# Kernel optimization log

Measured on AMD Instinct MI355X. Metric: run time of the kernel, lower is better.

Reference implementation:

```python
import jax, jax.numpy as jnp
import numpy as np

H = 16
EMB = 1024
DH = 64  # att_dim


def setup_inputs() -> dict:
    key = jax.random.key(0)
    k1, k2, k3 = jax.random.split(key, 3)
    B, T = 4, 2048
    x = jax.random.normal(k1, (B, T, EMB), dtype=jnp.float32)
    # torch nn.Linear weight layout: [out_features, in_features]
    w_qkv = jax.random.normal(k2, (3 * H * DH, EMB), dtype=jnp.float32) * (1.0 / np.sqrt(EMB))
    wo = jax.random.normal(k3, (EMB, H * DH), dtype=jnp.float32) * (1.0 / np.sqrt(H * DH))
    return {"x": x, "w_qkv": w_qkv, "wo": wo}


def reference(x, w_qkv, wo):
    B, T, C = x.shape
    qkv = jnp.einsum('btc,oc->bto', x, w_qkv)  # [B,T,3*H*DH]
    q, k, v = jnp.split(qkv, 3, axis=-1)
    # [B,H,T,DH]
    q = q.reshape(B, T, H, DH).transpose(0, 2, 1, 3)
    k = k.reshape(B, T, H, DH).transpose(0, 2, 1, 3)
    v = v.reshape(B, T, H, DH).transpose(0, 2, 1, 3)
    scale = 1.0 / np.sqrt(DH).astype(np.float32)
    scores = jnp.einsum('bhqd,bhkd->bhqk', q, k) * scale
    causal = jnp.tril(jnp.ones((T, T), dtype=bool))
    scores = jnp.where(causal, scores, jnp.finfo(scores.dtype).min)
    attn = jax.nn.softmax(scores, axis=-1)
    y = jnp.einsum('bhqk,bhkd->bhqd', attn, v)  # [B,H,T,DH]
    y = y.transpose(0, 2, 1, 3).reshape(B, T, H * DH)
    return jnp.einsum('bti,oi->bto', y, wo)
```

## Files before the change

kernel.cpp:

```cpp
#include <hip/hip_runtime.h>
#include <hip/hip_bf16.h>
#include <stdint.h>


typedef __attribute__((ext_vector_type(8))) short short8;
typedef __attribute__((ext_vector_type(4))) float floatx4;

extern "C" __device__ float __ocml_native_exp2_f32(float);

__device__ __forceinline__ ushort f2bf(float f) {
  uint32_t u = __float_as_uint(f);
  u += 0x7fff + ((u >> 16) & 1);
  return (ushort)(u >> 16);
}

#if __has_builtin(__builtin_amdgcn_cvt_pk_bf16_f32)
typedef __attribute__((ext_vector_type(2))) __bf16 bf16x2;
__device__ __forceinline__ uint32_t pack_bf16(float a, float b) {
  union { bf16x2 v; uint32_t u; } cv;
  cv.v = __builtin_amdgcn_cvt_pk_bf16_f32(a, b);
  return cv.u;
}
#else
__device__ __forceinline__ uint32_t pack_bf16(float a, float b) {
  uint32_t ua = __float_as_uint(a) + 0x8000u;
  uint32_t ub = __float_as_uint(b) + 0x8000u;
  return __builtin_amdgcn_perm(ub, ua, 0x07060302u);
}
#endif

__device__ __forceinline__ void gload16(const ushort* g, ushort* l) {
  __builtin_amdgcn_global_load_lds(
      (const __attribute__((address_space(1))) void*)g,
      (__attribute__((address_space(3))) void*)l, 16, 0, 0);
}

__global__ __launch_bounds__(256) void cvt3_kernel(const float* __restrict__ x,
                                                   const float* __restrict__ wq,
                                                   const float* __restrict__ wo,
                                                   ushort* __restrict__ xo,
                                                   ushort* __restrict__ wqo,
                                                   ushort* __restrict__ woo) {
  int i = blockIdx.x * 256 + threadIdx.x;
  const float* in; ushort* out; int idx;
  if (i < 2097152)      { in = x;  out = xo;  idx = i; }
  else if (i < 2883584) { in = wq; out = wqo; idx = i - 2097152; }
  else                  { in = wo; out = woo; idx = i - 2883584; }
  float4 v = ((const float4*)in)[idx];
  ushort4 o;
  o.x = f2bf(v.x); o.y = f2bf(v.y); o.z = f2bf(v.z); o.w = f2bf(v.w);
  ((ushort4*)out)[idx] = o;
}

template<int MODE>
__global__ __launch_bounds__(512) void gemm256(const ushort* __restrict__ A,
                                               const ushort* __restrict__ Bw,
                                               float* __restrict__ Cf,
                                               ushort* __restrict__ qb,
                                               ushort* __restrict__ kb,
                                               ushort* __restrict__ vt) {
  constexpr int SLOT = 12288;
  __shared__ ushort ring[4 * SLOT];
  int tid = threadIdx.x;
  int lane = tid & 63, wave = tid >> 6;
  int lrow = lane & 15, quad = lane >> 4;
  int wm = wave >> 1, wn = wave & 1;
  int wm64 = wm * 64, wn64 = wn * 64;
  int m0 = blockIdx.x * 256, n0 = blockIdx.y * 128;

  int srow = tid >> 2;
  int schunk8 = ((tid & 3) ^ ((tid >> 3) & 3)) * 8;
  const ushort* Ag0 = A + (size_t)(m0 + srow) * 1024 + schunk8;
  const ushort* Ag1 = Ag0 + (size_t)128 * 1024;
  const ushort* Bg0 = Bw + (size_t)(n0 + srow) * 1024 + schunk8;
  int fo2 = (quad ^ ((lrow >> 1) & 3)) * 8;

  const floatx4 zero4 = {0.f, 0.f, 0.f, 0.f};
  floatx4 acc[4][4];
#pragma unroll
  for (int i = 0; i < 4; i++)
#pragma unroll
    for (int j = 0; j < 4; j++) acc[i][j] = zero4;

  auto stage = [&](int t) {
    ushort* Sa = &ring[(t & 3) * SLOT];
    size_t kk = (size_t)t * 32;
    gload16(Ag0 + kk, &Sa[wave * 16 * 32]);
    gload16(Ag1 + kk, &Sa[(128 + wave * 16) * 32]);
    gload16(Bg0 + kk, &Sa[8192 + wave * 16 * 32]);
  };

  short8 fAa[4], fAb[4], fBa[4], fBb[4];

#define READF(u_, FN)                                                         \
  {                                                                           \
    ushort* As_ = &ring[((u_) & 3) * SLOT];                                   \
    ushort* Bs_ = As_ + 8192;                                                 \
    _Pragma("unroll")                                                         \
    for (int mi = 0; mi < 4; mi++)                                            \
      FN##a[mi] = *(const short8*)(&As_[(wm64 + mi * 16 + lrow) * 32 + fo2]); \
    _Pragma("unroll")                                                         \
    for (int nj = 0; nj < 4; nj++)                                            \
      FN##b[nj] = *(const short8*)(&Bs_[(wn64 + nj * 16 + lrow) * 32 + fo2]); \
  }

#define MFMAS(FC)                                                             \
  {                                                                           \
    __builtin_amdgcn_s_setprio(1);                                            \
    _Pragma("unroll")                                                         \
    for (int mi = 0; mi < 4; mi++)                                            \
      _Pragma("unroll")                                                       \
      for (int nj = 0; nj < 4; nj++)                                          \
        acc[mi][nj] = __builtin_amdgcn_mfma_f32_16x16x32_bf16(                \
            FC##a[mi], FC##b[nj], acc[mi][nj], 0, 0, 0);                      \
    __builtin_amdgcn_s_setprio(0);                                            \
  }

#define BARRIER(N_)                                                           \
  asm volatile("s_waitcnt vmcnt(" #N_ ")" ::: "memory");                      \
  __builtin_amdgcn_s_barrier();                                               \
  asm volatile("" ::: "memory");

#define KITER(u_, N_, ISSUE_, FC, FN)                                         \
  {                                                                           \
    BARRIER(N_)                                                               \
    READF(u_, FN)                                                             \
    if (ISSUE_) stage((u_) + 3);                                              \
    MFMAS(FC)                                                                 \
  }

  stage(0); stage(1); stage(2);
  BARRIER(6)
  READF(0, fA)
  stage(3);
#pragma unroll 1
  for (int p = 0; p < 14; ++p) {
    KITER(2 * p + 1, 6, true, fA, fB);
    KITER(2 * p + 2, 6, true, fB, fA);
  }
  KITER(29, 6, false, fA, fB);
  KITER(30, 3, false, fB, fA);
  KITER(31, 0, false, fA, fB);
  MFMAS(fB)

#undef KITER
#undef BARRIER
#undef MFMAS
#undef READF

  if (MODE == 1) {
#pragma unroll
    for (int mi = 0; mi < 4; mi++)
#pragma unroll
      for (int nj = 0; nj < 4; nj++)
#pragma unroll
        for (int r = 0; r < 4; r++) {
          int m = m0 + wm64 + mi * 16 + quad * 4 + r;
          int n = n0 + wn64 + nj * 16 + lrow;
          Cf[(size_t)m * 1024 + n] = acc[mi][nj][r];
        }
    return;
  }

  constexpr int CS = 136;
  ushort* sm = ring;
  int sec = n0 >> 10;
  int hrow = tid >> 4, kcol = tid & 15;
  __syncthreads();

  if (sec < 2) {
    float qs = (sec == 0) ? 0.18033688f : 1.0f;
    ushort* dst = (sec == 0) ? qb : kb;
    int hbase = n0 & 1023;
#pragma unroll 1
    for (int hf = 0; hf < 2; ++hf) {
      if ((wm >> 1) == hf) {
#pragma unroll
        for (int mi = 0; mi < 4; mi++)
#pragma unroll
          for (int nj = 0; nj < 4; nj++)
#pragma unroll
            for (int r = 0; r < 4; r++)
              sm[((wm & 1) * 64 + mi * 16 + quad * 4 + r) * CS +
                 wn64 + nj * 16 + lrow] = f2bf(acc[mi][nj][r] * qs);
      }
      __syncthreads();
#pragma unroll
      for (int mi = 0; mi < 4; mi++) {
        int mloc = mi * 32 + hrow;
        int m = m0 + hf * 128 + mloc, b_ = m >> 11, t = m & 2047;
        int col = kcol * 8;
        int h = (hbase + col) >> 6, d = col & 63;
        uint4 val = *(const uint4*)(&sm[mloc * CS + col]);
        *(uint4*)(dst + ((size_t)(b_ * 16 + h) * 2048 + t) * 64 + d) = val;
      }
      __syncthreads();
    }
  } else {
    int b_ = m0 >> 11, t0 = m0 & 2047;
#pragma unroll 1
    for (int hf = 0; hf < 2; ++hf) {
      if ((wm >> 1) == hf) {
#pragma unroll
        for (int mi = 0; mi < 4; mi++)
#pragma unroll
          for (int nj = 0; nj < 4; nj++) {
            uint2 w;
            w.x = pack_bf16(acc[mi][nj][0], acc[mi][nj][1]);
            w.y = pack_bf16(acc[mi][nj][2], acc[mi][nj][3]);
            *(uint2*)(&sm[(wn64 + nj * 16 + lrow) * CS +
                          (wm & 1) * 64 + mi * 16 + quad * 4]) = w;
          }
      }
      __syncthreads();
#pragma unroll
      for (int di = 0; di < 4; di++) {
        int nloc = di * 32 + hrow;
        int n = n0 + nloc, h = (n & 1023) >> 6, d = n & 63;
        uint4 val = *(const uint4*)(&sm[nloc * CS + kcol * 8]);
        *(uint4*)(vt + ((size_t)(b_ * 16 + h) * 64 + d) * 2048 +
                  t0 + hf * 128 + kcol * 8) = val;
      }
      __syncthreads();
    }
  }
}

__global__ __launch_bounds__(512) void attn_kernel(const ushort* __restrict__ qg,
                                                   const ushort* __restrict__ kg,
                                                   const ushort* __restrict__ vg,
                                                   ushort* __restrict__ y) {
  __shared__ ushort Ks[64 * 64];
  __shared__ ushort Vs[64 * 64];
  __shared__ ushort Ps[8 * 16 * 72];
  int tid = threadIdx.x;
  int lane = tid & 63, wave = tid >> 6;
  int lrow = lane & 15, quad = lane >> 4;
  int gx = blockIdx.x, gy = blockIdx.y;
  int pr = gy >> 3;
  int bh = (gy & 7) * 8 + gx;
  const ushort* qp = qg + (size_t)bh * 2048 * 64;
  const ushort* kp = kg + (size_t)bh * 2048 * 64;
  const ushort* vp = vg + (size_t)bh * 64 * 2048;
  int b = bh >> 4, h = bh & 15;
  int srow = tid >> 3, sc = tid & 7;
  int sswz = ((sc ^ (srow & 7)) * 8);
  int fo = (quad ^ (lrow & 7)) * 8;
  ushort* Pw = &Ps[wave * 16 * 72];

  const floatx4 zero4 = {0.f, 0.f, 0.f, 0.f};
  short8 ones;
#pragma unroll
  for (int i = 0; i < 8; i++) ones[i] = (short)0x3F80;

#pragma unroll 1
  for (int pass = 0; pass < 2; ++pass) {
    int qt = pass ? (15 - pr) : pr;
    int last = 2 * qt + 1;

    const ushort* qrow_p = qp + (size_t)((qt << 7) + wave * 16 + lrow) * 64;
    short8 a_q0 = *(const short8*)(qrow_p + quad * 8);
    short8 a_q1 = *(const short8*)(qrow_p + (quad ^ 4) * 8);

    uint4 kreg = *(const uint4*)(kp + (size_t)srow * 64 + sc * 8);
    uint4 vreg = *(const uint4*)(vp + (size_t)srow * 2048 + sc * 8);

    floatx4 l_acc = zero4;
    floatx4 o_acc[4];
#pragma unroll
    for (int j = 0; j < 4; j++) o_acc[j] = zero4;

#pragma unroll 1
    for (int kv = 0; kv <= last; kv++) {
      __syncthreads();
      *(uint4*)(&Ks[srow * 64 + sswz]) = kreg;
      *(uint4*)(&Vs[srow * 64 + sswz]) = vreg;
      if (kv < last) {
        kreg = *(const uint4*)(kp + (size_t)((kv + 1) * 64 + srow) * 64 + sc * 8);
        vreg = *(const uint4*)(vp + (size_t)srow * 2048 + (kv + 1) * 64 + sc * 8);
      }
      __syncthreads();

      floatx4 s[4];
#pragma unroll
      for (int ct = 0; ct < 4; ct++) {
        short8 k0 = *(const short8*)(&Ks[(ct * 16 + lrow) * 64 + fo]);
        short8 k1 = *(const short8*)(&Ks[(ct * 16 + lrow) * 64 + (fo ^ 32)]);
        floatx4 z = zero4;
        z = __builtin_amdgcn_mfma_f32_16x16x32_bf16(k0, a_q0, z, 0, 0, 0);
        z = __builtin_amdgcn_mfma_f32_16x16x32_bf16(k1, a_q1, z, 0, 0, 0);
        s[ct] = z;
      }

      if (kv >= 2 * qt) {
        int qabs = (qt << 7) + wave * 16 + lrow;
        int kbase = (kv << 6) + quad * 4;
#pragma unroll
        for (int ct = 0; ct < 4; ct++)
#pragma unroll
          for (int r = 0; r < 4; r++)
            if (kbase + ct * 16 + r > qabs) s[ct][r] = -1e30f;
      }

#pragma unroll
      for (int ct = 0; ct < 4; ct++) {
        float p0 = __ocml_native_exp2_f32(s[ct][0]);
        float p1 = __ocml_native_exp2_f32(s[ct][1]);
        float p2 = __ocml_native_exp2_f32(s[ct][2]);
        float p3 = __ocml_native_exp2_f32(s[ct][3]);
        uint2 w;
        w.x = pack_bf16(p0, p1);
        w.y = pack_bf16(p2, p3);
        *(uint2*)(&Pw[lrow * 72 + ct * 16 + quad * 4]) = w;
      }
      asm volatile("" ::: "memory");

      short8 a_p0 = *(const short8*)(&Pw[lrow * 72 + quad * 8]);
      short8 a_p1 = *(const short8*)(&Pw[lrow * 72 + 32 + quad * 8]);
      l_acc = __builtin_amdgcn_mfma_f32_16x16x32_bf16(a_p0, ones, l_acc, 0, 0, 0);
      l_acc = __builtin_amdgcn_mfma_f32_16x16x32_bf16(a_p1, ones, l_acc, 0, 0, 0);
#pragma unroll
      for (int j = 0; j < 4; j++) {
        short8 v0 = *(const short8*)(&Vs[(j * 16 + lrow) * 64 + fo]);
        short8 v1 = *(const short8*)(&Vs[(j * 16 + lrow) * 64 + (fo ^ 32)]);
        o_acc[j] = __builtin_amdgcn_mfma_f32_16x16x32_bf16(a_p0, v0, o_acc[j], 0, 0, 0);
        o_acc[j] = __builtin_amdgcn_mfma_f32_16x16x32_bf16(a_p1, v1, o_acc[j], 0, 0, 0);
      }
    }

    float inv[4];
#pragma unroll
    for (int r = 0; r < 4; r++) inv[r] = 1.0f / l_acc[r];

#pragma unroll
    for (int j = 0; j < 4; j++)
#pragma unroll
      for (int r = 0; r < 4; r++) {
        int t = (qt << 7) + wave * 16 + quad * 4 + r;
        y[((size_t)b * 2048 + t) * 1024 + h * 64 + j * 16 + lrow] =
            f2bf(o_acc[j][r] * inv[r]);
      }
  }
}

extern "C" void kernel_launch(void* const* d_in, const int* in_sizes, int n_in,
                              void* d_out, int out_size, void* d_ws, size_t ws_size,
                              hipStream_t stream) {
  const float* x     = (const float*)d_in[0];
  const float* w_qkv = (const float*)d_in[1];
  const float* wo    = (const float*)d_in[2];
  float* out = (float*)d_out;

  ushort* x_bf    = (ushort*)d_ws;
  ushort* wqkv_bf = x_bf + (size_t)8192 * 1024;
  ushort* wo_bf   = wqkv_bf + (size_t)3072 * 1024;
  ushort* qb      = wo_bf + (size_t)1024 * 1024;
  ushort* kb      = qb + (size_t)8388608;
  ushort* vt      = kb + (size_t)8388608;
  ushort* yb      = x_bf;

  cvt3_kernel<<<12288, 256, 0, stream>>>(x, w_qkv, wo, x_bf, wqkv_bf, wo_bf);
  gemm256<0><<<dim3(32, 24), 512, 0, stream>>>(x_bf, wqkv_bf, nullptr, qb, kb, vt);
  attn_kernel<<<dim3(8, 64), 512, 0, stream>>>(qb, kb, vt, yb);
  gemm256<1><<<dim3(32, 8), 512, 0, stream>>>(yb, wo_bf, out, nullptr, nullptr, nullptr);
}
```

Before: 227.1 us.

## Shrink QKV GEMM ring to three stages and use smaller-tile output projection GEMM

The QKV projection GEMM's shared-memory ring drops from four slots to three, with prefetch distance reduced from three to two stages, lowering LDS use per block. The output projection moves from the 256x128 templated GEMM (256 blocks) to a new 128x128, 256-thread kernel with a simple two-barrier K loop and 64-wide K tiles (512 blocks). This is meant to improve occupancy and CU fill for the smaller output GEMM. The cost is less latency hiding in the QKV GEMM and no software pipelining in the new kernel.

```diff
diff --git a/kernel.cpp b/kernel.cpp
--- a/kernel.cpp
+++ b/kernel.cpp
@@ -52,15 +52,13 @@
   ((ushort4*)out)[idx] = o;
 }
 
-template<int MODE>
 __global__ __launch_bounds__(512) void gemm256(const ushort* __restrict__ A,
                                                const ushort* __restrict__ Bw,
-                                               float* __restrict__ Cf,
                                                ushort* __restrict__ qb,
                                                ushort* __restrict__ kb,
                                                ushort* __restrict__ vt) {
   constexpr int SLOT = 12288;
-  __shared__ ushort ring[4 * SLOT];
+  __shared__ ushort ring[3 * SLOT];
   int tid = threadIdx.x;
   int lane = tid & 63, wave = tid >> 6;
   int lrow = lane & 15, quad = lane >> 4;
@@ -83,7 +81,7 @@
     for (int j = 0; j < 4; j++) acc[i][j] = zero4;
 
   auto stage = [&](int t) {
-    ushort* Sa = &ring[(t & 3) * SLOT];
+    ushort* Sa = &ring[(t % 3) * SLOT];
     size_t kk = (size_t)t * 32;
     gload16(Ag0 + kk, &Sa[wave * 16 * 32]);
     gload16(Ag1 + kk, &Sa[(128 + wave * 16) * 32]);
@@ -94,7 +92,7 @@
 
 #define READF(u_, FN)                                                         \
   {                                                                           \
-    ushort* As_ = &ring[((u_) & 3) * SLOT];                                   \
+    ushort* As_ = &ring[((u_) % 3) * SLOT];                                   \
     ushort* Bs_ = As_ + 8192;                                                 \
     _Pragma("unroll")                                                         \
     for (int mi = 0; mi < 4; mi++)                                            \
@@ -125,20 +123,20 @@
   {                                                                           \
     BARRIER(N_)                                                               \
     READF(u_, FN)                                                             \
-    if (ISSUE_) stage((u_) + 3);                                              \
+    if (ISSUE_) stage((u_) + 2);                                              \
     MFMAS(FC)                                                                 \
   }
 
-  stage(0); stage(1); stage(2);
-  BARRIER(6)
+  stage(0); stage(1);
+  BARRIER(3)
   READF(0, fA)
-  stage(3);
+  stage(2);
 #pragma unroll 1
   for (int p = 0; p < 14; ++p) {
-    KITER(2 * p + 1, 6, true, fA, fB);
-    KITER(2 * p + 2, 6, true, fB, fA);
-  }
-  KITER(29, 6, false, fA, fB);
+    KITER(2 * p + 1, 3, true, fA, fB);
+    KITER(2 * p + 2, 3, true, fB, fA);
+  }
+  KITER(29, 3, true, fA, fB);
   KITER(30, 3, false, fB, fA);
   KITER(31, 0, false, fA, fB);
   MFMAS(fB)
@@ -147,20 +145,6 @@
 #undef BARRIER
 #undef MFMAS
 #undef READF
-
-  if (MODE == 1) {
-#pragma unroll
-    for (int mi = 0; mi < 4; mi++)
-#pragma unroll
-      for (int nj = 0; nj < 4; nj++)
-#pragma unroll
-        for (int r = 0; r < 4; r++) {
-          int m = m0 + wm64 + mi * 16 + quad * 4 + r;
-          int n = n0 + wn64 + nj * 16 + lrow;
-          Cf[(size_t)m * 1024 + n] = acc[mi][nj][r];
-        }
-    return;
-  }
 
   constexpr int CS = 136;
   ushort* sm = ring;
@@ -224,6 +208,68 @@
       __syncthreads();
     }
   }
+}
+
+__global__ __launch_bounds__(256) void gemm_bt(const ushort* __restrict__ A,
+                                               const ushort* __restrict__ Bw,
+                                               float* __restrict__ Cf) {
+  __shared__ ushort smem[128 * 64 * 2];
+  ushort* As = smem;
+  ushort* Bs = smem + 128 * 64;
+  int tid = threadIdx.x;
+  int lane = tid & 63, wave = tid >> 6;
+  int lrow = lane & 15, quad = lane >> 4;
+  int wr = (wave >> 1) * 64, wc = (wave & 1) * 64;
+  int m0 = blockIdx.x * 128, n0 = blockIdx.y * 128;
+
+  const floatx4 zero4 = {0.f, 0.f, 0.f, 0.f};
+  floatx4 acc[4][4];
+#pragma unroll
+  for (int i = 0; i < 4; i++)
+#pragma unroll
+    for (int j = 0; j < 4; j++) acc[i][j] = zero4;
+
+  int rsub = tid >> 3;
+  int colb = (((tid & 7) ^ (rsub & 7)) * 8);
+  const ushort* Ag = A + (size_t)(m0 + rsub) * 1024 + colb;
+  const ushort* Bg = Bw + (size_t)(n0 + rsub) * 1024 + colb;
+  int fo = (quad ^ (lrow & 7)) * 8;
+
+  for (int kk = 0; kk < 1024; kk += 64) {
+    __syncthreads();
+#pragma unroll
+    for (int i = 0; i < 4; i++) {
+      gload16(Ag + kk + (size_t)i * 32 * 1024, &As[(8 * wave + 32 * i) * 64]);
+      gload16(Bg + kk + (size_t)i * 32 * 1024, &Bs[(8 * wave + 32 * i) * 64]);
+    }
+    __syncthreads();
+#pragma unroll
+    for (int ks = 0; ks < 2; ks++) {
+      short8 a[4], b[4];
+#pragma unroll
+      for (int i = 0; i < 4; i++)
+        a[i] = *(const short8*)(&As[(wr + i * 16 + lrow) * 64 + (fo ^ (32 * ks))]);
+#pragma unroll
+      for (int j = 0; j < 4; j++)
+        b[j] = *(const short8*)(&Bs[(wc + j * 16 + lrow) * 64 + (fo ^ (32 * ks))]);
+#pragma unroll
+      for (int i = 0; i < 4; i++)
+#pragma unroll
+        for (int j = 0; j < 4; j++)
+          acc[i][j] = __builtin_amdgcn_mfma_f32_16x16x32_bf16(a[i], b[j], acc[i][j], 0, 0, 0);
+    }
+  }
+
+#pragma unroll
+  for (int i = 0; i < 4; i++)
+#pragma unroll
+    for (int j = 0; j < 4; j++)
+#pragma unroll
+      for (int r = 0; r < 4; r++) {
+        int m = m0 + wr + i * 16 + quad * 4 + r;
+        int n = n0 + wc + j * 16 + lrow;
+        Cf[(size_t)m * 1024 + n] = acc[i][j][r];
+      }
 }
 
 __global__ __launch_bounds__(512) void attn_kernel(const ushort* __restrict__ qg,
@@ -360,7 +406,7 @@
   ushort* yb      = x_bf;
 
   cvt3_kernel<<<12288, 256, 0, stream>>>(x, w_qkv, wo, x_bf, wqkv_bf, wo_bf);
-  gemm256<0><<<dim3(32, 24), 512, 0, stream>>>(x_bf, wqkv_bf, nullptr, qb, kb, vt);
+  gemm256<<<dim3(32, 24), 512, 0, stream>>>(x_bf, wqkv_bf, qb, kb, vt);
   attn_kernel<<<dim3(8, 64), 512, 0, stream>>>(qb, kb, vt, yb);
-  gemm256<1><<<dim3(32, 8), 512, 0, stream>>>(yb, wo_bf, out, nullptr, nullptr, nullptr);
-}
+  gemm_bt<<<dim3(64, 8), 256, 0, stream>>>(yb, wo_bf, out);
+}
```

Result: no change. 224.8 us (-1.0%).
